# Kernel tuning notes

Measured on AMD Instinct MI355X. Metric: run time of the kernel, lower is better.

The kernel has to match this reference:

```python
import math
import jax, jax.numpy as jnp
import numpy as np

B, T, D = 8, 2048, 256
N_TICKS, DT, P_MIN, P_MAX = 3, 1.0, 2.0, 4.0


def setup_inputs() -> dict:
    key = jax.random.key(0)
    ks = jax.random.split(key, 16)
    s = 1.0 / math.sqrt(D)
    w = lambda k: jax.random.normal(k, (D, D), jnp.float32) * s
    zb = jnp.zeros((D,), jnp.float32)
    return {
        "z": jax.random.normal(ks[0], (B, T, D), jnp.float32),
        "in_w": w(ks[1]), "in_b": zb,
        "ln_g": jnp.ones((D,), jnp.float32), "ln_b": zb,
        "q_w": w(ks[2]), "q_b": zb,
        "k_w": w(ks[3]), "k_b": zb,
        "v_w": w(ks[4]), "v_b": zb,
        "o_w": w(ks[5]), "o_b": zb,
        "log_tau": jnp.zeros((D,), jnp.float32),
        "p1_w": w(ks[6]), "p1_b": zb,
        "p2_w": w(ks[7]), "p2_b": zb,
    }


def _layernorm(x, g, b, eps=1e-5):
    mu = jnp.mean(x, axis=-1, keepdims=True)
    var = jnp.var(x, axis=-1, keepdims=True)
    return (x - mu) * jax.lax.rsqrt(var + eps) * g + b


def _lin(x, w, b):
    return x @ w.T + b


def reference(z, in_w, in_b, ln_g, ln_b, q_w, q_b, k_w, k_b, v_w, v_b,
              o_w, o_b, log_tau, p1_w, p1_b, p2_w, p2_b):
    tau = jnp.exp(log_tau)  # [d]
    inv_sqrt_d = 1.0 / math.sqrt(D)
    uniform = 1.0 / T
    pred_losses, eff_ps = [], []
    for _ in range(N_TICKS):
        h = _layernorm(_lin(z, in_w, in_b), ln_g, ln_b)
        Q, K, V = _lin(h, q_w, q_b), _lin(h, k_w, k_b), _lin(h, v_w, v_b)
        sim = jnp.einsum('btd,bsd->bts', Q, K) * inv_sqrt_d  # [B,T,T]
        attn = jax.nn.softmax(sim, axis=-1)
        row_max = jnp.max(attn, axis=-1)  # [B,T]
        conf = (jnp.mean(row_max, axis=-1) - uniform) / (1.0 - uniform + 1e-6)
        conf = jnp.clip(conf, 0.0, 1.0)  # [B]
        eff_p = P_MIN + (P_MAX - P_MIN) * conf
        eff_ps.append(jax.lax.stop_gradient(eff_p))
        attn_sharp = jax.nn.softmax(sim * eff_p[:, None, None], axis=-1)
        context = jnp.einsum('bts,bsd->btd', attn_sharp, V)
        target = _lin(context, o_w, o_b)
        z_pred = _lin(jax.nn.relu(_lin(z, p1_w, p1_b)), p2_w, p2_b)
        dz = (target - z) / (tau + 1e-6)
        z_next = z + DT * dz
        pred_losses.append(jnp.mean((z_pred - jax.lax.stop_gradient(z_next)) ** 2))
        z = z_next
    pred_loss_mean = jnp.mean(jnp.stack(pred_losses))
    eff_p_mean = jnp.mean(jnp.concatenate(eff_ps))
    return z, pred_loss_mean, eff_p_mean
```

## Files before the change

### kernel.cpp

```cpp
#include <hip/hip_runtime.h>
#include <math.h>

#define Bn 8
#define Tn 2048
#define Dn 256
#define NTICK 3
#define NROWS (Bn*Tn)
#define ABM 64
#define NBLKA (NROWS/ABM)
#define BS 64
#define GM 64
#define NBLKG (NROWS/GM)
#define WP 65536

typedef unsigned int u32;
typedef unsigned short u16;
typedef __attribute__((ext_vector_type(8))) short bf16x8;
typedef __attribute__((ext_vector_type(4))) float f32x4;
typedef __attribute__((ext_vector_type(16))) float f32x16;

__device__ __forceinline__ float bf2f(u32 u){
  union { u32 i; float f; } x; x.i = u << 16; return x.f;
}
__device__ __forceinline__ u16 f2bf(float f){
  union { float f; u32 i; } x; x.f = f;
  u32 r = (x.i + 0x7fffu + ((x.i >> 16) & 1u)) >> 16;
  return (u16)r;
}
__device__ __forceinline__ void gld_lds16(const u16* gsrc, u16* ldst){
  __builtin_amdgcn_global_load_lds(
      (const __attribute__((address_space(1))) u32*)(const void*)gsrc,
      (__attribute__((address_space(3))) u32*)(void*)ldst, 16, 0, 0);
}

__device__ __forceinline__ void stage_A(const u16* __restrict__ A, int row0, char* smem){
  const int tid = threadIdx.x, lane = tid & 63, w = tid >> 6;
  #pragma unroll
  for (int r=0;r<8;++r){
    int s = w*16 + 2*r + (lane>>5);
    int slot = (lane & 31) ^ (s & 7);
    gld_lds16(A + (size_t)(row0 + s)*Dn + slot*8, (u16*)(smem + (w*16 + 2*r)*512));
  }
}
__device__ __forceinline__ void load_frags(const char* smem, bf16x8* af){
  const int tid = threadIdx.x, lane = tid & 63, w = tid >> 6;
  const int l7 = lane & 7, g = (lane >> 4) & 3, q15 = lane & 15;
  const char* ab = smem + (w*16 + q15)*512;
  #pragma unroll
  for (int kk=0;kk<8;++kk) af[kk] = *(const bf16x8*)(ab + 16*((4*kk+g)^l7));
}
__device__ __forceinline__ void stage_Wchunk(const u16* __restrict__ W, int c, char* wbuf){
  const int tid = threadIdx.x, lane = tid & 63, w = tid >> 6;
  #pragma unroll
  for (int r=0;r<2;++r){
    int rl = w*4 + 2*r + (lane>>5);
    int slot = (lane & 31) ^ (rl & 7);
    gld_lds16(W + (size_t)(c*16 + rl)*Dn + slot*8, (u16*)(wbuf + (w*4 + 2*r)*512));
  }
}
__device__ __forceinline__ void load_wfrags(const char* wbuf, bf16x8* wf){
  const int lane = threadIdx.x & 63;
  const int l7 = lane & 7, g = (lane >> 4) & 3, q15 = lane & 15;
  const char* wb_ = wbuf + q15*512;
  #pragma unroll
  for (int kk=0;kk<8;++kk) wf[kk] = *(const bf16x8*)(wb_ + 16*((4*kk+g)^l7));
}
__device__ __forceinline__ void zero_acc(f32x4* acc){
  #pragma unroll
  for (int nt=0;nt<16;++nt) acc[nt] = (f32x4){0.f,0.f,0.f,0.f};
}
#define CHUNK_STEP(c, NC, PLANE_OF, IDX_OF)                                    \
  asm volatile("s_waitcnt lgkmcnt(0)" ::: "memory");                           \
  if ((c) < (NC)-2) { asm volatile("s_waitcnt vmcnt(2)" ::: "memory"); }       \
  else              { asm volatile("s_waitcnt vmcnt(0)" ::: "memory"); }       \
  __builtin_amdgcn_sched_barrier(0);                                           \
  __builtin_amdgcn_s_barrier();                                                \
  if ((c)+3 < (NC)) stage_Wchunk(PLANE_OF((c)+3), IDX_OF((c)+3), ring + (((c)+3)&3)*8192);

__global__ void k_prep(const float* __restrict__ s0, const float* __restrict__ s1,
                       const float* __restrict__ s2, const float* __restrict__ s3,
                       const float* __restrict__ s4, const float* __restrict__ s5,
                       const float* __restrict__ s6, u16* __restrict__ dst){
  int y = blockIdx.y;
  const float* s = (y==0)?s0:(y==1)?s1:(y==2)?s2:(y==3)?s3:(y==4)?s4:(y==5)?s5:s6;
  int i = (blockIdx.x*256 + threadIdx.x)*4;
  float4 v = *(const float4*)(s + i);
  u16 h0=f2bf(v.x), h1=f2bf(v.y), h2=f2bf(v.z), h3=f2bf(v.w);
  uint2 hi, lo;
  hi.x = (u32)h0 | ((u32)h1 << 16);
  hi.y = (u32)h2 | ((u32)h3 << 16);
  lo.x = (u32)f2bf(v.x - bf2f(h0)) | ((u32)f2bf(v.y - bf2f(h1)) << 16);
  lo.y = (u32)f2bf(v.z - bf2f(h2)) | ((u32)f2bf(v.w - bf2f(h3)) << 16);
  *(uint2*)(dst + (size_t)y*WP + i) = hi;
  *(uint2*)(dst + (size_t)(7+y)*WP + i) = lo;
}

__global__ void k_split(const float* __restrict__ s, u16* __restrict__ dh, u16* __restrict__ dl,
                        float* __restrict__ stats){
  if (blockIdx.x == 0 && threadIdx.x < 64) stats[threadIdx.x] = 0.f;
  int i = (blockIdx.x*256 + threadIdx.x)*4;
  float4 v = *(const float4*)(s + i);
  u16 h0=f2bf(v.x), h1=f2bf(v.y), h2=f2bf(v.z), h3=f2bf(v.w);
  uint2 hi, lo;
  hi.x = (u32)h0 | ((u32)h1 << 16);
  hi.y = (u32)h2 | ((u32)h3 << 16);
  lo.x = (u32)f2bf(v.x - bf2f(h0)) | ((u32)f2bf(v.y - bf2f(h1)) << 16);
  lo.y = (u32)f2bf(v.z - bf2f(h2)) | ((u32)f2bf(v.w - bf2f(h3)) << 16);
  *(uint2*)(dh + i) = hi;
  *(uint2*)(dl + i) = lo;
}

__global__ __launch_bounds__(256) void k_gemm_ln(
    const u16* __restrict__ Ahi, const u16* __restrict__ Alo,
    const u16* __restrict__ Whi, const u16* __restrict__ Wlo,
    const float* __restrict__ bias, const float* __restrict__ gamma, const float* __restrict__ beta,
    u16* __restrict__ h)
{
  __shared__ __align__(16) char smem[65536];
  char* ring = smem;
  f32x4 acc[16];
  const int row0 = blockIdx.x * GM;
  stage_A(Ahi, row0, smem);
  stage_A(Alo, row0, smem + 32768);
  asm volatile("s_waitcnt vmcnt(0)" ::: "memory");
  __builtin_amdgcn_sched_barrier(0);
  bf16x8 afh[8], afl[8];
  load_frags(smem, afh);
  load_frags(smem + 32768, afl);
  asm volatile("s_waitcnt lgkmcnt(0)" ::: "memory");
  __builtin_amdgcn_sched_barrier(0);
  __builtin_amdgcn_s_barrier();
  zero_acc(acc);
  #define LN_PL(i) ((i) < 16 ? Whi : Wlo)
  #define LN_IX(i) ((i) & 15)
  stage_Wchunk(LN_PL(0), LN_IX(0), ring + 0*8192);
  stage_Wchunk(LN_PL(1), LN_IX(1), ring + 1*8192);
  stage_Wchunk(LN_PL(2), LN_IX(2), ring + 2*8192);
  asm volatile("s_waitcnt vmcnt(4)" ::: "memory");
  __builtin_amdgcn_sched_barrier(0);
  __builtin_amdgcn_s_barrier();
  for (int c=0; c<32; ++c){
    bf16x8 wf[8];
    load_wfrags(ring + (c&3)*8192, wf);
    int nt = c & 15;
    if (c < 16){
      #pragma unroll
      for (int kk=0;kk<8;++kk)
        acc[nt] = __builtin_amdgcn_mfma_f32_16x16x32_bf16(afh[kk], wf[kk], acc[nt], 0,0,0);
      #pragma unroll
      for (int kk=0;kk<8;++kk)
        acc[nt] = __builtin_amdgcn_mfma_f32_16x16x32_bf16(afl[kk], wf[kk], acc[nt], 0,0,0);
    } else {
      #pragma unroll
      for (int kk=0;kk<8;++kk)
        acc[nt] = __builtin_amdgcn_mfma_f32_16x16x32_bf16(afh[kk], wf[kk], acc[nt], 0,0,0);
    }
    CHUNK_STEP(c, 32, LN_PL, LN_IX)
  }
  const int tid = threadIdx.x, lane = tid & 63, w = tid >> 6;
  const int g4 = lane >> 4, q15 = lane & 15;
  float bcol[16], gcol[16], becol[16];
  #pragma unroll
  for (int nt=0;nt<16;++nt){
    int col = nt*16 + q15;
    bcol[nt] = bias[col]; gcol[nt] = gamma[col]; becol[nt] = beta[col];
  }
  float mu[4], rstd[4];
  #pragma unroll
  for (int j=0;j<4;++j){
    float s=0.f, q=0.f;
    #pragma unroll
    for (int nt=0;nt<16;++nt){ float v = acc[nt][j] + bcol[nt]; s += v; q += v*v; }
    #pragma unroll
    for (int off=1; off<16; off<<=1){ s += __shfl_xor(s,off); q += __shfl_xor(q,off); }
    float m = s*(1.f/Dn);
    mu[j] = m; rstd[j] = rsqrtf(q*(1.f/Dn) - m*m + 1e-5f);
  }
  const size_t rbase = (size_t)(row0 + w*16 + g4*4);
  #pragma unroll
  for (int nt=0;nt<16;++nt){
    #pragma unroll
    for (int j=0;j<4;++j){
      float v = (acc[nt][j] + bcol[nt] - mu[j])*rstd[j]*gcol[nt] + becol[nt];
      h[(rbase+j)*Dn + nt*16 + q15] = f2bf(v);
    }
  }
}

__global__ __launch_bounds__(256) void k_gemm_qkv(
    const u16* __restrict__ h, const u16* __restrict__ wbf,
    const float* __restrict__ qb, const float* __restrict__ kb, const float* __restrict__ vb,
    u16* __restrict__ Qo, u16* __restrict__ Ko, u16* __restrict__ Vo)
{
  const u16 *Whi, *Wlo; const float* bias; u16* out;
  if (blockIdx.y == 0){ Whi = wbf + 1*WP; Wlo = wbf + 8*WP;  bias = qb; out = Qo; }
  else if (blockIdx.y == 1){ Whi = wbf + 2*WP; Wlo = wbf + 9*WP;  bias = kb; out = Ko; }
  else { Whi = wbf + 3*WP; Wlo = wbf + 10*WP; bias = vb; out = Vo; }
  __shared__ __align__(16) char smem[65536];
  char* ring = smem + 32768;
  f32x4 acc[16];
  const int row0 = blockIdx.x * GM;
  stage_A(h, row0, smem);
  #define QK_PL(i) ((i) < 16 ? Whi : Wlo)
  #define QK_IX(i) ((i) & 15)
  stage_Wchunk(QK_PL(0), QK_IX(0), ring + 0*8192);
  stage_Wchunk(QK_PL(1), QK_IX(1), ring + 1*8192);
  stage_Wchunk(QK_PL(2), QK_IX(2), ring + 2*8192);
  asm volatile("s_waitcnt vmcnt(4)" ::: "memory");
  __builtin_amdgcn_sched_barrier(0);
  bf16x8 af[8];
  load_frags(smem, af);
  zero_acc(acc);
  __builtin_amdgcn_s_barrier();
  for (int c=0; c<32; ++c){
    bf16x8 wf[8];
    load_wfrags(ring + (c&3)*8192, wf);
    int nt = c & 15;
    #pragma unroll
    for (int kk=0;kk<8;++kk)
      acc[nt] = __builtin_amdgcn_mfma_f32_16x16x32_bf16(af[kk], wf[kk], acc[nt], 0,0,0);
    CHUNK_STEP(c, 32, QK_PL, QK_IX)
  }
  const int tid = threadIdx.x, lane = tid & 63, w = tid >> 6;
  const int g4 = lane >> 4, q15 = lane & 15;
  const size_t rbase = (size_t)(row0 + w*16 + g4*4);
  #pragma unroll
  for (int nt=0;nt<16;++nt){
    float bc = bias[nt*16 + q15];
    #pragma unroll
    for (int j=0;j<4;++j)
      out[(rbase+j)*Dn + nt*16 + q15] = f2bf(acc[nt][j] + bc);
  }
}

__global__ __launch_bounds__(256) void k_gemm_update(
    const u16* __restrict__ Chi, const u16* __restrict__ Clo,
    const u16* __restrict__ Whi, const u16* __restrict__ Wlo,
    const float* __restrict__ ob,
    const u16* __restrict__ zhi_old, const u16* __restrict__ zlo_old,
    const float* __restrict__ log_tau,
    u16* __restrict__ zhi_new, u16* __restrict__ zlo_new,
    float* __restrict__ zout)
{
  __shared__ __align__(16) char smem[65536];
  char* ring = smem;
  f32x4 acc[16];
  const int row0 = blockIdx.x * GM;
  stage_A(Chi, row0, smem);
  stage_A(Clo, row0, smem + 32768);
  asm volatile("s_waitcnt vmcnt(0)" ::: "memory");
  __builtin_amdgcn_sched_barrier(0);
  bf16x8 afh[8], afl[8];
  load_frags(smem, afh);
  load_frags(smem + 32768, afl);
  asm volatile("s_waitcnt lgkmcnt(0)" ::: "memory");
  __builtin_amdgcn_sched_barrier(0);
  __builtin_amdgcn_s_barrier();
  zero_acc(acc);
  stage_Wchunk(LN_PL(0), LN_IX(0), ring + 0*8192);
  stage_Wchunk(LN_PL(1), LN_IX(1), ring + 1*8192);
  stage_Wchunk(LN_PL(2), LN_IX(2), ring + 2*8192);
  asm volatile("s_waitcnt vmcnt(4)" ::: "memory");
  __builtin_amdgcn_sched_barrier(0);
  __builtin_amdgcn_s_barrier();
  for (int c=0; c<32; ++c){
    bf16x8 wf[8];
    load_wfrags(ring + (c&3)*8192, wf);
    int nt = c & 15;
    if (c < 16){
      #pragma unroll
      for (int kk=0;kk<8;++kk)
        acc[nt] = __builtin_amdgcn_mfma_f32_16x16x32_bf16(afh[kk], wf[kk], acc[nt], 0,0,0);
      #pragma unroll
      for (int kk=0;kk<8;++kk)
        acc[nt] = __builtin_amdgcn_mfma_f32_16x16x32_bf16(afl[kk], wf[kk], acc[nt], 0,0,0);
    } else {
      #pragma unroll
      for (int kk=0;kk<8;++kk)
        acc[nt] = __builtin_amdgcn_mfma_f32_16x16x32_bf16(afh[kk], wf[kk], acc[nt], 0,0,0);
    }
    CHUNK_STEP(c, 32, LN_PL, LN_IX)
  }
  const int tid = threadIdx.x, lane = tid & 63, w = tid >> 6;
  const int g4 = lane >> 4, q15 = lane & 15;
  const size_t rbase = (size_t)(row0 + w*16 + g4*4);
  #pragma unroll
  for (int nt=0;nt<16;++nt){
    int col = nt*16 + q15;
    float bc = ob[col];
    float invt = 1.f/(expf(log_tau[col]) + 1e-6f);
    #pragma unroll
    for (int j=0;j<4;++j){
      size_t idx = (rbase+j)*Dn + col;
      float zo = bf2f(zhi_old[idx]) + bf2f(zlo_old[idx]);
      float zn = zo + (acc[nt][j] + bc - zo)*invt;
      u16 zh = f2bf(zn);
      zhi_new[idx] = zh;
      zlo_new[idx] = f2bf(zn - bf2f(zh));
      if (zout) zout[idx] = zn;
    }
  }
}

__global__ __launch_bounds__(256) void k_gemm_relu(
    const u16* __restrict__ A, const u16* __restrict__ Wb, const float* __restrict__ bias,
    u16* __restrict__ t1)
{
  __shared__ __align__(16) char smem[65536];
  char* ring = smem + 32768;
  f32x4 acc[16];
  const int row0 = blockIdx.x * GM;
  stage_A(A, row0, smem);
  #define W1_PL(i) (Wb)
  #define W1_IX(i) (i)
  stage_Wchunk(Wb, 0, ring + 0*8192);
  stage_Wchunk(Wb, 1, ring + 1*8192);
  stage_Wchunk(Wb, 2, ring + 2*8192);
  asm volatile("s_waitcnt vmcnt(4)" ::: "memory");
  __builtin_amdgcn_sched_barrier(0);
  bf16x8 af[8];
  load_frags(smem, af);
  zero_acc(acc);
  __builtin_amdgcn_s_barrier();
  for (int c=0; c<16; ++c){
    bf16x8 wf[8];
    load_wfrags(ring + (c&3)*8192, wf);
    #pragma unroll
    for (int kk=0;kk<8;++kk)
      acc[c] = __builtin_amdgcn_mfma_f32_16x16x32_bf16(af[kk], wf[kk], acc[c], 0,0,0);
    CHUNK_STEP(c, 16, W1_PL, W1_IX)
  }
  const int tid = threadIdx.x, lane = tid & 63, w = tid >> 6;
  const int g4 = lane >> 4, q15 = lane & 15;
  const size_t rbase = (size_t)(row0 + w*16 + g4*4);
  #pragma unroll
  for (int nt=0;nt<16;++nt){
    float bc = bias[nt*16 + q15];
    #pragma unroll
    for (int j=0;j<4;++j)
      t1[(rbase+j)*Dn + nt*16 + q15] = f2bf(fmaxf(acc[nt][j] + bc, 0.f));
  }
}

__global__ __launch_bounds__(256) void k_gemm_loss(
    const u16* __restrict__ t1, const u16* __restrict__ Wb, const float* __restrict__ bias,
    const u16* __restrict__ zhi_new, const u16* __restrict__ zlo_new,
    float* __restrict__ loss_acc)
{
  __shared__ __align__(16) char smem[65536];
  __shared__ float red[4];
  char* ring = smem + 32768;
  f32x4 acc[16];
  const int row0 = blockIdx.x * GM;
  stage_A(t1, row0, smem);
  stage_Wchunk(Wb, 0, ring + 0*8192);
  stage_Wchunk(Wb, 1, ring + 1*8192);
  stage_Wchunk(Wb, 2, ring + 2*8192);
  asm volatile("s_waitcnt vmcnt(4)" ::: "memory");
  __builtin_amdgcn_sched_barrier(0);
  bf16x8 af[8];
  load_frags(smem, af);
  zero_acc(acc);
  __builtin_amdgcn_s_barrier();
  for (int c=0; c<16; ++c){
    bf16x8 wf[8];
    load_wfrags(ring + (c&3)*8192, wf);
    #pragma unroll
    for (int kk=0;kk<8;++kk)
      acc[c] = __builtin_amdgcn_mfma_f32_16x16x32_bf16(af[kk], wf[kk], acc[c], 0,0,0);
    CHUNK_STEP(c, 16, W1_PL, W1_IX)
  }
  const int tid = threadIdx.x, lane = tid & 63, w = tid >> 6;
  const int g4 = lane >> 4, q15 = lane & 15;
  const size_t rbase = (size_t)(row0 + w*16 + g4*4);
  float lsum = 0.f;
  #pragma unroll
  for (int nt=0;nt<16;++nt){
    float bc = bias[nt*16 + q15];
    #pragma unroll
    for (int j=0;j<4;++j){
      size_t idx = (rbase+j)*Dn + nt*16 + q15;
      float zn = bf2f(zhi_new[idx]) + bf2f(zlo_new[idx]);
      float dn = acc[nt][j] + bc - zn;
      lsum += dn*dn;
    }
  }
  #pragma unroll
  for (int off=1; off<64; off<<=1) lsum += __shfl_xor(lsum, off);
  if (lane == 0) red[w] = lsum;
  __syncthreads();
  if (tid == 0) atomicAdd(loss_acc, red[0]+red[1]+red[2]+red[3]);
}

__global__ __launch_bounds__(256) void k_passA(
    const u16* __restrict__ Qg, const u16* __restrict__ Kg,
    float* __restrict__ conf_b)
{
  __shared__ __align__(16) char smem[65536];
  const int tid = threadIdx.x;
  const int lane = tid & 63, w = tid >> 6;
  const int l31 = lane & 31, hi5 = lane >> 5;
  const int qh = w >> 1, sh = w & 1;
  const int row0 = blockIdx.x * ABM;
  const int b = row0 >> 11;
  const size_t kbase = (size_t)b * Tn * Dn;

  #pragma unroll
  for (int r=0;r<8;++r){
    int s = w*16 + 2*r + (lane>>5);
    int slot = (lane & 31) ^ (s & 7);
    gld_lds16(Qg + (size_t)(row0 + s)*Dn + slot*8, (u16*)(smem + (w*16 + 2*r)*512));
  }
  asm volatile("s_waitcnt vmcnt(0)" ::: "memory");
  __builtin_amdgcn_sched_barrier(0);
  __builtin_amdgcn_s_barrier();
  bf16x8 qf[16];
  {
    const char* qb = smem + (qh*32 + l31)*512;
    const int r7 = l31 & 7;
    #pragma unroll
    for (int t=0;t<16;++t) qf[t] = *(const bf16x8*)(qb + 16*((2*t+hi5)^r7));
  }
  asm volatile("s_waitcnt lgkmcnt(0)" ::: "memory");
  __builtin_amdgcn_sched_barrier(0);
  __builtin_amdgcn_s_barrier();
  #pragma unroll
  for (int r=0;r<8;++r){
    int s = w*16 + 2*r + (lane>>5);
    int slot = (lane & 31) ^ (s & 7);
    gld_lds16(Kg + kbase + (size_t)(s)*Dn + slot*8, (u16*)(smem + 32768 + (w*16 + 2*r)*512));
  }
  #pragma unroll
  for (int r=0;r<8;++r){
    int s = w*16 + 2*r + (lane>>5);
    int slot = (lane & 31) ^ (s & 7);
    gld_lds16(Kg + kbase + (size_t)(BS + s)*Dn + slot*8, (u16*)(smem + (w*16 + 2*r)*512));
  }
  asm volatile("s_waitcnt vmcnt(8)" ::: "memory");
  __builtin_amdgcn_sched_barrier(0);
  __builtin_amdgcn_s_barrier();

  float m_run = -INFINITY, l_run = 0.f;
  const int sr7 = l31 & 7;
  int cur = 1;
  for (int tile=0; tile<Tn/BS; ++tile){
    const char* kb = smem + cur*32768 + (sh*32 + l31)*512;
    f32x16 sc = (f32x16)(0.f);
    #pragma unroll
    for (int t=0;t<16;++t){
      bf16x8 kf = *(const bf16x8*)(kb + 16*((2*t+hi5)^sr7));
      sc = __builtin_amdgcn_mfma_f32_32x32x16_bf16(kf, qf[t], sc, 0,0,0);
    }
    float vmax = -INFINITY;
    float vals[16];
    #pragma unroll
    for (int i=0;i<16;++i){ float v = sc[i]*0.0625f; vals[i]=v; vmax=fmaxf(vmax,v); }
    vmax = fmaxf(vmax, __shfl_xor(vmax,32));
    float mnew = fmaxf(m_run, vmax);
    float corr = __expf(m_run - mnew);
    float esum = 0.f;
    #pragma unroll
    for (int i=0;i<16;++i) esum += __expf(vals[i]-mnew);
    esum += __shfl_xor(esum,32);
    l_run = l_run*corr + esum;
    m_run = mnew;

    asm volatile("s_waitcnt vmcnt(0)" ::: "memory");
    __builtin_amdgcn_sched_barrier(0);
    __builtin_amdgcn_s_barrier();
    if (tile < Tn/BS - 2){
      #pragma unroll
      for (int r=0;r<8;++r){
        int s = w*16 + 2*r + (lane>>5);
        int slot = (lane & 31) ^ (s & 7);
        gld_lds16(Kg + kbase + (size_t)((tile+2)*BS + s)*Dn + slot*8,
                  (u16*)(smem + cur*32768 + (w*16 + 2*r)*512));
      }
    }
    cur ^= 1;
  }
  __syncthreads();
  if (sh == 1 && lane < 32){
    float2 ml; ml.x = m_run; ml.y = l_run;
    *(float2*)(smem + (qh*32 + l31)*8) = ml;
  }
  __syncthreads();
  if (sh == 0){
    float2 o = *(const float2*)(smem + (qh*32 + l31)*8);
    float m2 = fmaxf(m_run, o.x);
    float lm = l_run*__expf(m_run - m2) + o.y*__expf(o.x - m2);
    float r1 = 1.f/lm;
    #pragma unroll
    for (int off=1; off<64; off<<=1) r1 += __shfl_xor(r1, off);
    if (lane==0) atomicAdd(conf_b + b, r1*0.5f);
  }
}

#define KB0 0
#define KB1 32768
#define VT0 65536
#define VT1 98304
#define PST 131072
__global__ __launch_bounds__(512) void k_passB(
    const u16* __restrict__ Qg, const u16* __restrict__ Kg, const u16* __restrict__ Vg,
    const float* __restrict__ conf_sum, u16* __restrict__ Chi, u16* __restrict__ Clo)
{
  __shared__ __align__(16) char smem[139264];
  const int tid = threadIdx.x;
  const int lane = tid & 63, w = tid >> 6;
  const int qg = w & 3, hs = w >> 2;
  const int l7 = lane & 7, g = (lane >> 4) & 3, q15 = lane & 15;
  const int row0 = blockIdx.x * ABM;
  const int b = row0 >> 11;
  const size_t kbase = (size_t)b * Tn * Dn;
  float mean_rm = conf_sum[b] * (1.f/Tn);
  float uniform = 1.f/Tn;
  float conf = fminf(fmaxf((mean_rm - uniform)/(1.f - uniform + 1e-6f), 0.f), 1.f);
  const float scale = (2.f + 2.f*conf) * 0.0625f;
  const int tid2 = tid & 255;
  const int dblk = tid2 >> 3, sblk = tid2 & 7;
  uint4 vreg[8];
  const int NT = Tn/BS;

  if (hs == 0){
    #pragma unroll
    for (int r=0;r<8;++r){
      int s = w*16 + 2*r + (lane>>5);
      int slot = (lane & 31) ^ (s & 7);
      gld_lds16(Qg + (size_t)(row0 + s)*Dn + slot*8, (u16*)(smem + KB0 + (w*16 + 2*r)*512));
    }
  } else {
    const u16* vsrc = Vg + kbase + (size_t)(sblk*8)*Dn + dblk*8;
    #pragma unroll
    for (int si=0; si<8; ++si) vreg[si] = *(const uint4*)(vsrc + (size_t)si*Dn);
  }
  __syncthreads();
  bf16x8 qf[8];
  {
    const char* qb = smem + KB0 + (qg*16 + q15)*512;
    #pragma unroll
    for (int kk=0;kk<8;++kk) qf[kk] = *(const bf16x8*)(qb + 16*((4*kk+g)^l7));
  }
  __syncthreads();
  if (hs == 0){
    #pragma unroll
    for (int r=0;r<8;++r){
      int s = w*16 + 2*r + (lane>>5);
      int slot = (lane & 31) ^ (s & 7);
      gld_lds16(Kg + kbase + (size_t)(s)*Dn + slot*8, (u16*)(smem + KB0 + (w*16 + 2*r)*512));
    }
    #pragma unroll
    for (int r=0;r<8;++r){
      int s = w*16 + 2*r + (lane>>5);
      int slot = (lane & 31) ^ (s & 7);
      gld_lds16(Kg + kbase + (size_t)(BS + s)*Dn + slot*8, (u16*)(smem + KB1 + (w*16 + 2*r)*512));
    }
    asm volatile("s_waitcnt vmcnt(8)" ::: "memory");
    __builtin_amdgcn_sched_barrier(0);
  } else {
    const u32* rw = (const u32*)vreg;
    #pragma unroll
    for (int dl=0; dl<8; ++dl){
      int wi = dl >> 1;
      u32 sel = (dl & 1) ? 0x07060302u : 0x05040100u;
      uint4 o;
      o.x = __builtin_amdgcn_perm(rw[1*4+wi], rw[0*4+wi], sel);
      o.y = __builtin_amdgcn_perm(rw[3*4+wi], rw[2*4+wi], sel);
      o.z = __builtin_amdgcn_perm(rw[5*4+wi], rw[4*4+wi], sel);
      o.w = __builtin_amdgcn_perm(rw[7*4+wi], rw[6*4+wi], sel);
      int d = dblk*8 + dl;
      *(uint4*)(smem + VT0 + d*128 + 16*(sblk ^ dl)) = o;
    }
    asm volatile("s_waitcnt lgkmcnt(0)" ::: "memory");
    __builtin_amdgcn_sched_barrier(0);
  }
  __builtin_amdgcn_s_barrier();

  float m_run = -INFINITY, l_run = 0.f;
  f32x4 oa[16];
  #pragma unroll
  for (int md=0;md<16;++md) oa[md] = (f32x4){0.f,0.f,0.f,0.f};

  char* pbase = smem + PST + w*1024 + q15*64;
  const int psw = q15 & 3;

  int cur = 0;
  for (int tile=0; tile<NT; ++tile){
    const char* kbuf = smem + (cur ? KB1 : KB0);
    const char* vbuf = smem + (cur ? VT1 : VT0);
    char* vbuf_n = (char*)smem + (cur ? VT0 : VT1);
    if (hs == 1 && tile < NT-1){
      const u16* vsrc = Vg + kbase + (size_t)((tile+1)*BS + sblk*8)*Dn + dblk*8;
      #pragma unroll
      for (int si=0; si<8; ++si) vreg[si] = *(const uint4*)(vsrc + (size_t)si*Dn);
    }
    f32x4 sc[2];
    sc[0] = (f32x4){0.f,0.f,0.f,0.f};
    sc[1] = (f32x4){0.f,0.f,0.f,0.f};
    #pragma unroll
    for (int kk=0;kk<8;++kk){
      #pragma unroll
      for (int msl=0;msl<2;++msl){
        int msg = 2*hs + msl;
        bf16x8 kf = *(const bf16x8*)(kbuf + (msg*16+q15)*512 + 16*((4*kk+g)^l7));
        sc[msl] = __builtin_amdgcn_mfma_f32_16x16x32_bf16(kf, qf[kk], sc[msl], 0,0,0);
      }
    }
    float vmax = -INFINITY;
    float vals[8];
    #pragma unroll
    for (int msl=0;msl<2;++msl){
      #pragma unroll
      for (int j=0;j<4;++j){ float v = sc[msl][j]*scale; vals[msl*4+j]=v; vmax=fmaxf(vmax,v); }
    }
    vmax = fmaxf(vmax, __shfl_xor(vmax,16));
    vmax = fmaxf(vmax, __shfl_xor(vmax,32));
    float mnew = fmaxf(m_run, vmax);
    float corr = __expf(m_run - mnew);
    float esum = 0.f;
    #pragma unroll
    for (int t2=0;t2<8;++t2){ float p = __expf(vals[t2]-mnew); vals[t2]=p; esum += p; }
    esum += __shfl_xor(esum,16); esum += __shfl_xor(esum,32);
    l_run = l_run*corr + esum;
    m_run = mnew;
    #pragma unroll
    for (int md=0;md<16;++md) oa[md] *= corr;
    #pragma unroll
    for (int msl=0;msl<2;++msl){
      uint2 pw;
      pw.x = (u32)f2bf(vals[msl*4+0]) | ((u32)f2bf(vals[msl*4+1]) << 16);
      pw.y = (u32)f2bf(vals[msl*4+2]) | ((u32)f2bf(vals[msl*4+3]) << 16);
      int slot = (2*msl + (g>>1)) ^ psw;
      *(uint2*)(pbase + slot*16 + (g&1)*8) = pw;
    }
    asm volatile("s_waitcnt lgkmcnt(0)" ::: "memory");
    __builtin_amdgcn_sched_barrier(0);
    {
      bf16x8 pf = *(const bf16x8*)(pbase + ((g ^ psw)*16));
      #pragma unroll
      for (int md=0; md<16; ++md){
        bf16x8 vf = *(const bf16x8*)(vbuf + (md*16+q15)*128 + 16*((4*hs+g)^l7));
        oa[md] = __builtin_amdgcn_mfma_f32_16x16x32_bf16(vf, pf, oa[md], 0,0,0);
      }
    }
    if (hs == 1){
      if (tile < NT-1){
        asm volatile("s_waitcnt vmcnt(0)" ::: "memory");
        __builtin_amdgcn_sched_barrier(0);
        const u32* rw = (const u32*)vreg;
        #pragma unroll
        for (int dl=0; dl<8; ++dl){
          int wi = dl >> 1;
          u32 sel = (dl & 1) ? 0x07060302u : 0x05040100u;
          uint4 o;
          o.x = __builtin_amdgcn_perm(rw[1*4+wi], rw[0*4+wi], sel);
          o.y = __builtin_amdgcn_perm(rw[3*4+wi], rw[2*4+wi], sel);
          o.z = __builtin_amdgcn_perm(rw[5*4+wi], rw[4*4+wi], sel);
          o.w = __builtin_amdgcn_perm(rw[7*4+wi], rw[6*4+wi], sel);
          int d = dblk*8 + dl;
          *(uint4*)(vbuf_n + d*128 + 16*(sblk ^ dl)) = o;
        }
      }
      asm volatile("s_waitcnt lgkmcnt(0)" ::: "memory");
    } else {
      asm volatile("s_waitcnt vmcnt(0) lgkmcnt(0)" ::: "memory");
    }
    __builtin_amdgcn_sched_barrier(0);
    __builtin_amdgcn_s_barrier();
    if (hs == 0 && tile < NT-2){
      #pragma unroll
      for (int r=0;r<8;++r){
        int s = w*16 + 2*r + (lane>>5);
        int slot = (lane & 31) ^ (s & 7);
        gld_lds16(Kg + kbase + (size_t)((tile+2)*BS + s)*Dn + slot*8,
                  (u16*)(smem + (cur ? KB1 : KB0) + (w*16 + 2*r)*512));
      }
    }
    cur ^= 1;
  }
  __syncthreads();
  if (hs == 1){
    char* ob_ = smem + (qg*64 + lane)*256;
    #pragma unroll
    for (int md=0; md<16; ++md)
      *(f32x4*)(ob_ + (md ^ q15)*16) = oa[md];
    float2 ml; ml.x = m_run; ml.y = l_run;
    *(float2*)(smem + VT0 + (qg*64 + lane)*8) = ml;
  }
  __syncthreads();
  if (hs == 0){
    float2 ml = *(const float2*)(smem + VT0 + (qg*64 + lane)*8);
    float m = fmaxf(m_run, ml.x);
    float ca = __expf(m_run - m), cb = __expf(ml.x - m);
    float l = l_run*ca + ml.y*cb;
    float inv = 1.f / l;
    const char* ob_ = smem + (qg*64 + lane)*256;
    const size_t rr = (size_t)(row0 + qg*16 + q15)*Dn + g*4;
    #pragma unroll
    for (int md=0; md<16; ++md){
      f32x4 ob = *(const f32x4*)(ob_ + (md ^ q15)*16);
      float v0 = (oa[md][0]*ca + ob[0]*cb)*inv;
      float v1 = (oa[md][1]*ca + ob[1]*cb)*inv;
      float v2 = (oa[md][2]*ca + ob[2]*cb)*inv;
      float v3 = (oa[md][3]*ca + ob[3]*cb)*inv;
      uint2 hi, lo;
      u16 h0=f2bf(v0), h1=f2bf(v1), h2=f2bf(v2), h3=f2bf(v3);
      hi.x = (u32)h0 | ((u32)h1 << 16);
      hi.y = (u32)h2 | ((u32)h3 << 16);
      lo.x = (u32)f2bf(v0 - bf2f(h0)) | ((u32)f2bf(v1 - bf2f(h1)) << 16);
      lo.y = (u32)f2bf(v2 - bf2f(h2)) | ((u32)f2bf(v3 - bf2f(h3)) << 16);
      *(uint2*)(Chi + rr + md*16) = hi;
      *(uint2*)(Clo + rr + md*16) = lo;
    }
  }
}

__global__ void k_finalize(const float* __restrict__ loss3, const float* __restrict__ conf_sum,
                           float* __restrict__ out_scalars){
  if (threadIdx.x == 0){
    float ls = (loss3[0]+loss3[1]+loss3[2]) * (1.f/(3.f*NROWS*Dn));
    float es = 0.f;
    float uniform = 1.f/Tn;
    #pragma unroll
    for (int i=0;i<NTICK*Bn;++i){
      float mean_rm = conf_sum[i] * (1.f/Tn);
      float conf = fminf(fmaxf((mean_rm - uniform)/(1.f - uniform + 1e-6f), 0.f), 1.f);
      es += 2.f + 2.f*conf;
    }
    out_scalars[0] = ls;
    out_scalars[1] = es * (1.f/(NTICK*Bn));
  }
}

extern "C" void kernel_launch(void* const* d_in, const int* in_sizes, int n_in,
                              void* d_out, int out_size, void* d_ws, size_t ws_size,
                              hipStream_t stream) {
  (void)in_sizes; (void)n_in; (void)out_size; (void)ws_size;
  const float* z_in   = (const float*)d_in[0];
  const float* in_w   = (const float*)d_in[1];
  const float* in_b   = (const float*)d_in[2];
  const float* ln_g   = (const float*)d_in[3];
  const float* ln_b   = (const float*)d_in[4];
  const float* q_w    = (const float*)d_in[5];
  const float* q_b    = (const float*)d_in[6];
  const float* k_w    = (const float*)d_in[7];
  const float* k_b    = (const float*)d_in[8];
  const float* v_w    = (const float*)d_in[9];
  const float* v_b    = (const float*)d_in[10];
  const float* o_w    = (const float*)d_in[11];
  const float* o_b    = (const float*)d_in[12];
  const float* log_tau= (const float*)d_in[13];
  const float* p1_w   = (const float*)d_in[14];
  const float* p1_b   = (const float*)d_in[15];
  const float* p2_w   = (const float*)d_in[16];
  const float* p2_b   = (const float*)d_in[17];

  float* out = (float*)d_out;
  const size_t NE = (size_t)NROWS * Dn;

  u16*  zh0  = (u16*)d_ws;
  u16*  zl0  = zh0 + NE;
  u16*  zh1  = zl0 + NE;
  u16*  zl1  = zh1 + NE;
  u16*  hbuf = zl1 + NE;
  u16*  Qb   = hbuf + NE;
  u16*  Kb   = Qb + NE;
  u16*  Vb   = Kb + NE;
  u16*  Chi  = Vb + NE;
  u16*  Clo  = Chi + NE;
  u16*  t1b  = Clo + NE;
  u16*  wbf  = t1b + NE;
  float* stats = (float*)(wbf + 14*WP);
  float* conf_sum = stats;
  float* loss     = stats + 24;

  k_prep<<<dim3(64,7), 256, 0, stream>>>(in_w, q_w, k_w, v_w, o_w, p1_w, p2_w, wbf);
  k_split<<<4096, 256, 0, stream>>>(z_in, zh0, zl0, stats);

  u16* zh_list[2] = { zh0, zh1 };
  u16* zl_list[2] = { zl0, zl1 };

  for (int t = 0; t < NTICK; ++t){
    u16* zh_old = zh_list[t & 1];
    u16* zl_old = zl_list[t & 1];
    u16* zh_new = zh_list[(t+1) & 1];
    u16* zl_new = zl_list[(t+1) & 1];
    float* zout = (t == NTICK-1) ? out : nullptr;
    k_gemm_ln<<<NBLKG, 256, 0, stream>>>(zh_old, zl_old, wbf + 0*WP, wbf + 7*WP,
                                         in_b, ln_g, ln_b, hbuf);
    k_gemm_qkv<<<dim3(NBLKG,3), 256, 0, stream>>>(hbuf, wbf, q_b, k_b, v_b, Qb, Kb, Vb);
    k_passA<<<NBLKA, 256, 0, stream>>>(Qb, Kb, conf_sum + t*8);
    k_passB<<<NBLKA, 512, 0, stream>>>(Qb, Kb, Vb, conf_sum + t*8, Chi, Clo);
    k_gemm_update<<<NBLKG, 256, 0, stream>>>(Chi, Clo, wbf + 4*WP, wbf + 11*WP, o_b,
                                             zh_old, zl_old, log_tau, zh_new, zl_new, zout);
    k_gemm_relu<<<NBLKG, 256, 0, stream>>>(zh_old, wbf + 5*WP, p1_b, t1b);
    k_gemm_loss<<<NBLKG, 256, 0, stream>>>(t1b, wbf + 6*WP, p2_b, zh_new, zl_new, loss + t);
  }
  k_finalize<<<1, 64, 0, stream>>>(loss, conf_sum, out + NE);
}
```

Measured before the change: 764.8 us.

## Reuse pass-A row maxima to drop online softmax rescaling in pass B

```diff
diff --git a/kernel.cpp b/kernel.cpp
--- a/kernel.cpp
+++ b/kernel.cpp
@@ -394,7 +394,7 @@
 
 __global__ __launch_bounds__(256) void k_passA(
     const u16* __restrict__ Qg, const u16* __restrict__ Kg,
-    float* __restrict__ conf_b)
+    float* __restrict__ conf_b, float* __restrict__ mrow)
 {
   __shared__ __align__(16) char smem[65536];
   const int tid = threadIdx.x;
@@ -489,6 +489,7 @@
     float2 o = *(const float2*)(smem + (qh*32 + l31)*8);
     float m2 = fmaxf(m_run, o.x);
     float lm = l_run*__expf(m_run - m2) + o.y*__expf(o.x - m2);
+    if (lane < 32) mrow[row0 + qh*32 + l31] = m2;
     float r1 = 1.f/lm;
     #pragma unroll
     for (int off=1; off<64; off<<=1) r1 += __shfl_xor(r1, off);
@@ -496,16 +497,15 @@
   }
 }
 
-#define KB0 0
-#define KB1 32768
-#define VT0 65536
-#define VT1 98304
-#define PST 131072
-__global__ __launch_bounds__(512) void k_passB(
+#define KBF 0
+#define VBF 32768
+#define PST 65536
+__global__ __launch_bounds__(512, 4) void k_passB(
     const u16* __restrict__ Qg, const u16* __restrict__ Kg, const u16* __restrict__ Vg,
-    const float* __restrict__ conf_sum, u16* __restrict__ Chi, u16* __restrict__ Clo)
+    const float* __restrict__ conf_sum, const float* __restrict__ mrow,
+    u16* __restrict__ Chi, u16* __restrict__ Clo)
 {
-  __shared__ __align__(16) char smem[139264];
+  __shared__ __align__(16) char smem[73728];
   const int tid = threadIdx.x;
   const int lane = tid & 63, w = tid >> 6;
   const int qg = w & 3, hs = w >> 2;
@@ -517,9 +517,10 @@
   float uniform = 1.f/Tn;
   float conf = fminf(fmaxf((mean_rm - uniform)/(1.f - uniform + 1e-6f), 0.f), 1.f);
   const float scale = (2.f + 2.f*conf) * 0.0625f;
+  const float mfix = mrow[row0 + qg*16 + q15] * scale * 16.f;
   const int tid2 = tid & 255;
   const int dblk = tid2 >> 3, sblk = tid2 & 7;
-  uint4 vreg[8];
+  uint4 kreg[8], vreg[8];
   const int NT = Tn/BS;
 
   if (hs == 0){
@@ -527,7 +528,13 @@
     for (int r=0;r<8;++r){
       int s = w*16 + 2*r + (lane>>5);
       int slot = (lane & 31) ^ (s & 7);
-      gld_lds16(Qg + (size_t)(row0 + s)*Dn + slot*8, (u16*)(smem + KB0 + (w*16 + 2*r)*512));
+      gld_lds16(Qg + (size_t)(row0 + s)*Dn + slot*8, (u16*)(smem + KBF + (w*16 + 2*r)*512));
+    }
+    #pragma unroll
+    for (int r=0;r<8;++r){
+      int s = w*16 + 2*r + (lane>>5);
+      int slot = (lane & 31) ^ (s & 7);
+      kreg[r] = *(const uint4*)(Kg + kbase + (size_t)s*Dn + slot*8);
     }
   } else {
     const u16* vsrc = Vg + kbase + (size_t)(sblk*8)*Dn + dblk*8;
@@ -537,26 +544,21 @@
   __syncthreads();
   bf16x8 qf[8];
   {
-    const char* qb = smem + KB0 + (qg*16 + q15)*512;
+    const char* qb = smem + KBF + (qg*16 + q15)*512;
     #pragma unroll
     for (int kk=0;kk<8;++kk) qf[kk] = *(const bf16x8*)(qb + 16*((4*kk+g)^l7));
   }
   __syncthreads();
   if (hs == 0){
+    #pragma unroll
+    for (int r=0;r<8;++r)
+      *(uint4*)(smem + KBF + (w*16 + 2*r)*512 + lane*16) = kreg[r];
     #pragma unroll
     for (int r=0;r<8;++r){
       int s = w*16 + 2*r + (lane>>5);
       int slot = (lane & 31) ^ (s & 7);
-      gld_lds16(Kg + kbase + (size_t)(s)*Dn + slot*8, (u16*)(smem + KB0 + (w*16 + 2*r)*512));
-    }
-    #pragma unroll
-    for (int r=0;r<8;++r){
-      int s = w*16 + 2*r + (lane>>5);
-      int slot = (lane & 31) ^ (s & 7);
-      gld_lds16(Kg + kbase + (size_t)(BS + s)*Dn + slot*8, (u16*)(smem + KB1 + (w*16 + 2*r)*512));
-    }
-    asm volatile("s_waitcnt vmcnt(8)" ::: "memory");
-    __builtin_amdgcn_sched_barrier(0);
+      kreg[r] = *(const uint4*)(Kg + kbase + (size_t)(BS + s)*Dn + slot*8);
+    }
   } else {
     const u32* rw = (const u32*)vreg;
     #pragma unroll
@@ -569,14 +571,17 @@
       o.z = __builtin_amdgcn_perm(rw[5*4+wi], rw[4*4+wi], sel);
       o.w = __builtin_amdgcn_perm(rw[7*4+wi], rw[6*4+wi], sel);
       int d = dblk*8 + dl;
-      *(uint4*)(smem + VT0 + d*128 + 16*(sblk ^ dl)) = o;
-    }
-    asm volatile("s_waitcnt lgkmcnt(0)" ::: "memory");
-    __builtin_amdgcn_sched_barrier(0);
-  }
-  __builtin_amdgcn_s_barrier();
-
-  float m_run = -INFINITY, l_run = 0.f;
+      *(uint4*)(smem + VBF + d*128 + 16*(sblk ^ dl)) = o;
+    }
+    const u16* vsrc = Vg + kbase + (size_t)(BS + sblk*8)*Dn + dblk*8;
+    #pragma unroll
+    for (int si=0; si<8; ++si) vreg[si] = *(const uint4*)(vsrc + (size_t)si*Dn);
+  }
+  asm volatile("s_waitcnt lgkmcnt(0)" ::: "memory");
+  __builtin_amdgcn_sched_barrier(0);
+  __builtin_amdgcn_s_barrier();
+
+  float l_run = 0.f;
   f32x4 oa[16];
   #pragma unroll
   for (int md=0;md<16;++md) oa[md] = (f32x4){0.f,0.f,0.f,0.f};
@@ -584,16 +589,7 @@
   char* pbase = smem + PST + w*1024 + q15*64;
   const int psw = q15 & 3;
 
-  int cur = 0;
   for (int tile=0; tile<NT; ++tile){
-    const char* kbuf = smem + (cur ? KB1 : KB0);
-    const char* vbuf = smem + (cur ? VT1 : VT0);
-    char* vbuf_n = (char*)smem + (cur ? VT0 : VT1);
-    if (hs == 1 && tile < NT-1){
-      const u16* vsrc = Vg + kbase + (size_t)((tile+1)*BS + sblk*8)*Dn + dblk*8;
-      #pragma unroll
-      for (int si=0; si<8; ++si) vreg[si] = *(const uint4*)(vsrc + (size_t)si*Dn);
-    }
     f32x4 sc[2];
     sc[0] = (f32x4){0.f,0.f,0.f,0.f};
     sc[1] = (f32x4){0.f,0.f,0.f,0.f};
@@ -602,29 +598,22 @@
       #pragma unroll
       for (int msl=0;msl<2;++msl){
         int msg = 2*hs + msl;
-        bf16x8 kf = *(const bf16x8*)(kbuf + (msg*16+q15)*512 + 16*((4*kk+g)^l7));
+        bf16x8 kf = *(const bf16x8*)(smem + KBF + (msg*16+q15)*512 + 16*((4*kk+g)^l7));
         sc[msl] = __builtin_amdgcn_mfma_f32_16x16x32_bf16(kf, qf[kk], sc[msl], 0,0,0);
       }
     }
-    float vmax = -INFINITY;
     float vals[8];
+    float esum = 0.f;
     #pragma unroll
     for (int msl=0;msl<2;++msl){
       #pragma unroll
-      for (int j=0;j<4;++j){ float v = sc[msl][j]*scale; vals[msl*4+j]=v; vmax=fmaxf(vmax,v); }
-    }
-    vmax = fmaxf(vmax, __shfl_xor(vmax,16));
-    vmax = fmaxf(vmax, __shfl_xor(vmax,32));
-    float mnew = fmaxf(m_run, vmax);
-    float corr = __expf(m_run - mnew);
-    float esum = 0.f;
-    #pragma unroll
-    for (int t2=0;t2<8;++t2){ float p = __expf(vals[t2]-mnew); vals[t2]=p; esum += p; }
+      for (int j=0;j<4;++j){
+        float p = __expf(sc[msl][j]*scale - mfix);
+        vals[msl*4+j] = p; esum += p;
+      }
+    }
     esum += __shfl_xor(esum,16); esum += __shfl_xor(esum,32);
-    l_run = l_run*corr + esum;
-    m_run = mnew;
-    #pragma unroll
-    for (int md=0;md<16;++md) oa[md] *= corr;
+    l_run += esum;
     #pragma unroll
     for (int msl=0;msl<2;++msl){
       uint2 pw;
@@ -639,14 +628,29 @@
       bf16x8 pf = *(const bf16x8*)(pbase + ((g ^ psw)*16));
       #pragma unroll
       for (int md=0; md<16; ++md){
-        bf16x8 vf = *(const bf16x8*)(vbuf + (md*16+q15)*128 + 16*((4*hs+g)^l7));
+        bf16x8 vf = *(const bf16x8*)(smem + VBF + (md*16+q15)*128 + 16*((4*hs+g)^l7));
         oa[md] = __builtin_amdgcn_mfma_f32_16x16x32_bf16(vf, pf, oa[md], 0,0,0);
       }
     }
-    if (hs == 1){
-      if (tile < NT-1){
-        asm volatile("s_waitcnt vmcnt(0)" ::: "memory");
-        __builtin_amdgcn_sched_barrier(0);
+    asm volatile("s_waitcnt lgkmcnt(0)" ::: "memory");
+    __builtin_amdgcn_sched_barrier(0);
+    __builtin_amdgcn_s_barrier();
+    if (tile < NT-1){
+      asm volatile("s_waitcnt vmcnt(0)" ::: "memory");
+      __builtin_amdgcn_sched_barrier(0);
+      if (hs == 0){
+        #pragma unroll
+        for (int r=0;r<8;++r)
+          *(uint4*)(smem + KBF + (w*16 + 2*r)*512 + lane*16) = kreg[r];
+        if (tile < NT-2){
+          #pragma unroll
+          for (int r=0;r<8;++r){
+            int s = w*16 + 2*r + (lane>>5);
+            int slot = (lane & 31) ^ (s & 7);
+            kreg[r] = *(const uint4*)(Kg + kbase + (size_t)((tile+2)*BS + s)*Dn + slot*8);
+          }
+        }
+      } else {
         const u32* rw = (const u32*)vreg;
         #pragma unroll
         for (int dl=0; dl<8; ++dl){
@@ -658,25 +662,18 @@
           o.z = __builtin_amdgcn_perm(rw[5*4+wi], rw[4*4+wi], sel);
           o.w = __builtin_amdgcn_perm(rw[7*4+wi], rw[6*4+wi], sel);
           int d = dblk*8 + dl;
-          *(uint4*)(vbuf_n + d*128 + 16*(sblk ^ dl)) = o;
+          *(uint4*)(smem + VBF + d*128 + 16*(sblk ^ dl)) = o;
+        }
+        if (tile < NT-2){
+          const u16* vsrc = Vg + kbase + (size_t)((tile+2)*BS + sblk*8)*Dn + dblk*8;
+          #pragma unroll
+          for (int si=0; si<8; ++si) vreg[si] = *(const uint4*)(vsrc + (size_t)si*Dn);
         }
       }
       asm volatile("s_waitcnt lgkmcnt(0)" ::: "memory");
-    } else {
-      asm volatile("s_waitcnt vmcnt(0) lgkmcnt(0)" ::: "memory");
-    }
-    __builtin_amdgcn_sched_barrier(0);
+      __builtin_amdgcn_sched_barrier(0);
+    }
     __builtin_amdgcn_s_barrier();
-    if (hs == 0 && tile < NT-2){
-      #pragma unroll
-      for (int r=0;r<8;++r){
-        int s = w*16 + 2*r + (lane>>5);
-        int slot = (lane & 31) ^ (s & 7);
-        gld_lds16(Kg + kbase + (size_t)((tile+2)*BS + s)*Dn + slot*8,
-                  (u16*)(smem + (cur ? KB1 : KB0) + (w*16 + 2*r)*512));
-      }
-    }
-    cur ^= 1;
   }
   __syncthreads();
   if (hs == 1){
@@ -684,25 +681,21 @@
     #pragma unroll
     for (int md=0; md<16; ++md)
       *(f32x4*)(ob_ + (md ^ q15)*16) = oa[md];
-    float2 ml; ml.x = m_run; ml.y = l_run;
-    *(float2*)(smem + VT0 + (qg*64 + lane)*8) = ml;
+    *(float*)(smem + PST + (qg*64 + lane)*4) = l_run;
   }
   __syncthreads();
   if (hs == 0){
-    float2 ml = *(const float2*)(smem + VT0 + (qg*64 + lane)*8);
-    float m = fmaxf(m_run, ml.x);
-    float ca = __expf(m_run - m), cb = __expf(ml.x - m);
-    float l = l_run*ca + ml.y*cb;
-    float inv = 1.f / l;
+    float lo_ = *(const float*)(smem + PST + (qg*64 + lane)*4);
+    float inv = 1.f / (l_run + lo_);
     const char* ob_ = smem + (qg*64 + lane)*256;
     const size_t rr = (size_t)(row0 + qg*16 + q15)*Dn + g*4;
     #pragma unroll
     for (int md=0; md<16; ++md){
       f32x4 ob = *(const f32x4*)(ob_ + (md ^ q15)*16);
-      float v0 = (oa[md][0]*ca + ob[0]*cb)*inv;
-      float v1 = (oa[md][1]*ca + ob[1]*cb)*inv;
-      float v2 = (oa[md][2]*ca + ob[2]*cb)*inv;
-      float v3 = (oa[md][3]*ca + ob[3]*cb)*inv;
+      float v0 = (oa[md][0] + ob[0])*inv;
+      float v1 = (oa[md][1] + ob[1])*inv;
+      float v2 = (oa[md][2] + ob[2])*inv;
+      float v3 = (oa[md][3] + ob[3])*inv;
       uint2 hi, lo;
       u16 h0=f2bf(v0), h1=f2bf(v1), h2=f2bf(v2), h3=f2bf(v3);
       hi.x = (u32)h0 | ((u32)h1 << 16);
@@ -773,6 +766,7 @@
   float* stats = (float*)(wbf + 14*WP);
   float* conf_sum = stats;
   float* loss     = stats + 24;
+  float* mrowb    = stats + 64;
 
   k_prep<<<dim3(64,7), 256, 0, stream>>>(in_w, q_w, k_w, v_w, o_w, p1_w, p2_w, wbf);
   k_split<<<4096, 256, 0, stream>>>(z_in, zh0, zl0, stats);
@@ -789,8 +783,8 @@
     k_gemm_ln<<<NBLKG, 256, 0, stream>>>(zh_old, zl_old, wbf + 0*WP, wbf + 7*WP,
                                          in_b, ln_g, ln_b, hbuf);
     k_gemm_qkv<<<dim3(NBLKG,3), 256, 0, stream>>>(hbuf, wbf, q_b, k_b, v_b, Qb, Kb, Vb);
-    k_passA<<<NBLKA, 256, 0, stream>>>(Qb, Kb, conf_sum + t*8);
-    k_passB<<<NBLKA, 512, 0, stream>>>(Qb, Kb, Vb, conf_sum + t*8, Chi, Clo);
+    k_passA<<<NBLKA, 256, 0, stream>>>(Qb, Kb, conf_sum + t*8, mrowb);
+    k_passB<<<NBLKA, 512, 0, stream>>>(Qb, Kb, Vb, conf_sum + t*8, mrowb, Chi, Clo);
     k_gemm_update<<<NBLKG, 256, 0, stream>>>(Chi, Clo, wbf + 4*WP, wbf + 11*WP, o_b,
                                              zh_old, zl_old, log_tau, zh_new, zl_new, zout);
     k_gemm_relu<<<NBLKG, 256, 0, stream>>>(zh_old, wbf + 5*WP, p1_b, t1b);
```

Measured after the change: 1.677 ms. +119.3%, slower.
